# Optimization experiments

Hardware: AMD Instinct MI355X
Metric: run time of the kernel (lower is better)

## Reference

```python
import jax, jax.numpy as jnp
import numpy as np

D_X, D_K, D_V = 1024, 128, 128
B, N = 8, 2048


def setup_inputs() -> dict:
    key = jax.random.key(0)
    ks = jax.random.split(key, 7)
    s = lambda fan_in: 1.0 / np.sqrt(fan_in)
    return {
        "x": jax.random.normal(ks[0], (B, N, D_X), dtype=jnp.float32),
        "w_q": jax.random.uniform(ks[1], (D_K, D_X), jnp.float32, -s(D_X), s(D_X)),
        "b_q": jax.random.uniform(ks[2], (D_K,), jnp.float32, -s(D_X), s(D_X)),
        "w_k": jax.random.uniform(ks[3], (D_K, D_X), jnp.float32, -s(D_X), s(D_X)),
        "b_k": jax.random.uniform(ks[4], (D_K,), jnp.float32, -s(D_X), s(D_X)),
        "w_v": jax.random.uniform(ks[5], (D_V, D_X), jnp.float32, -s(D_X), s(D_X)),
        "b_v": jax.random.uniform(ks[6], (D_V,), jnp.float32, -s(D_X), s(D_X)),
    }


def reference(x, w_q, b_q, w_k, b_k, w_v, b_v):
    # Q is computed in the original module but unused; omit (no effect on output).
    K = jnp.einsum('bnx,kx->bnk', x, w_k) + b_k  # [B,N,d_k]
    V = jnp.einsum('bnx,vx->bnv', x, w_v) + b_v  # [B,N,d_v]
    # logits = K @ V^T / sqrt(d_k)  -> [B,N,N]  (note: K vs V, not Q vs K)
    scale = 1.0 / np.sqrt(D_K).astype(np.float32)
    logits = jnp.einsum('bnk,bmk->bnm', K, V) * scale
    attn = jax.nn.softmax(logits, axis=-1)
    return jnp.einsum('bnm,bmv->bnv', attn, V)
```

## Files before the change

### kernel.cpp

```cpp
#include <hip/hip_runtime.h>
#include <hip/hip_bf16.h>


typedef short s16x8 __attribute__((ext_vector_type(8)));
typedef float f32x4 __attribute__((ext_vector_type(4)));
typedef unsigned short u16;

#define AS1 __attribute__((address_space(1)))
#define AS3 __attribute__((address_space(3)))

__device__ __forceinline__ void gld_lds16(const void* g, void* l) {
  __builtin_amdgcn_global_load_lds((const AS1 unsigned int*)g, (AS3 unsigned int*)l, 16, 0, 0);
}

__device__ __forceinline__ float bf2f(u16 u) {
  unsigned int v = ((unsigned int)u) << 16;
  return __builtin_bit_cast(float, v);
}
__device__ __forceinline__ u16 f2bf(float f) {
  unsigned int u = __builtin_bit_cast(unsigned int, f);
  u += 0x7fffu + ((u >> 16) & 1u);
  return (u16)(u >> 16);
}
__device__ __forceinline__ unsigned pack_bf2(float a, float b) {
  unsigned ua = __builtin_bit_cast(unsigned, a) + 0x8000u;
  unsigned ub = __builtin_bit_cast(unsigned, b) + 0x8000u;
  return __builtin_amdgcn_perm(ub, ua, 0x07060302u);
}

__global__ __launch_bounds__(256, 4) void wconv_kernel(
    const float* __restrict__ wk, const float* __restrict__ wv,
    u16* __restrict__ wbf)
{
  const int e = (blockIdx.x * 256 + threadIdx.x) * 8;
  const float* src = (e < 131072) ? (wk + e) : (wv + (e - 131072));
  float4 a = *(const float4*)src;
  float4 b = *(const float4*)(src + 4);
  union { unsigned u[4]; s16x8 v; } pk;
  pk.u[0] = pack_bf2(a.x, a.y); pk.u[1] = pack_bf2(a.z, a.w);
  pk.u[2] = pack_bf2(b.x, b.y); pk.u[3] = pack_bf2(b.z, b.w);
  *(s16x8*)(wbf + e) = pk.v;
}

__global__ __launch_bounds__(256, 2) void kv_gemm_kernel(
    const float* __restrict__ x, const u16* __restrict__ wbf,
    const float* __restrict__ bk, const float* __restrict__ bv,
    u16* __restrict__ Kout, u16* __restrict__ Vout, u16* __restrict__ VTout)
{
  __shared__ u16 sA[2][4 * 512];
  __shared__ u16 sB[2][32 * 512];

  const int tid  = threadIdx.x;
  const int wave = tid >> 6;
  const int lane = tid & 63;
  const int l16  = lane & 15;
  const int lq   = lane >> 4;
  const int row0 = blockIdx.x * 32;

  f32x4 acc[2][4];
  for (int i = 0; i < 2; ++i)
    for (int j = 0; j < 4; ++j) acc[i][j] = (f32x4){0.f, 0.f, 0.f, 0.f};

  const int kc = tid & 7, arow = tid >> 3;
  const float* aSrc = x + (size_t)(row0 + arow) * 1024 + kc * 8;
  const int aSlot = ((((arow >> 4) * 2 + (kc >> 2)) * 64) + (kc & 3) * 16 + (arow & 15)) * 8;

  const u16* bSrc[8];
  for (int i = 0; i < 8; ++i) {
    const int sl = wave + i * 4;
    bSrc[i] = wbf + (size_t)((sl >> 1) * 16 + l16) * 1024 + (sl & 1) * 32 + lq * 8;
  }

  float4 p0a = *(const float4*)(aSrc);
  float4 p0b = *(const float4*)(aSrc + 4);
  float4 p1a = *(const float4*)(aSrc + 64);
  float4 p1b = *(const float4*)(aSrc + 68);
  for (int i = 0; i < 8; ++i)
    gld_lds16(bSrc[i], &sB[0][(wave + i * 4) * 512]);

  for (int s = 0; s < 16; ++s) {
    const int buf = s & 1;
    {
      union { unsigned u[4]; s16x8 v; } pk;
      pk.u[0] = pack_bf2(p0a.x, p0a.y); pk.u[1] = pack_bf2(p0a.z, p0a.w);
      pk.u[2] = pack_bf2(p0b.x, p0b.y); pk.u[3] = pack_bf2(p0b.z, p0b.w);
      *(s16x8*)(&sA[buf][aSlot]) = pk.v;
    }
    __syncthreads();
    if (s + 1 < 16)
      for (int i = 0; i < 8; ++i)
        gld_lds16(bSrc[i] + (s + 1) * 64, &sB[buf ^ 1][(wave + i * 4) * 512]);
    p0a = p1a; p0b = p1b;
    if (s + 2 < 16) {
      p1a = *(const float4*)(aSrc + (s + 2) * 64);
      p1b = *(const float4*)(aSrc + (s + 2) * 64 + 4);
    }
    s16x8 af[2][2], bf[4][2];
    for (int rb = 0; rb < 2; ++rb)
      for (int ks = 0; ks < 2; ++ks)
        af[rb][ks] = *(const s16x8*)(&sA[buf][((rb * 2 + ks) * 64 + lane) * 8]);
    for (int cb = 0; cb < 4; ++cb)
      for (int ks = 0; ks < 2; ++ks)
        bf[cb][ks] = *(const s16x8*)(&sB[buf][(((wave * 4 + cb) * 2 + ks) * 64 + lane) * 8]);
    for (int rb = 0; rb < 2; ++rb)
      for (int cb = 0; cb < 4; ++cb)
        for (int ks = 0; ks < 2; ++ks)
          acc[rb][cb] = __builtin_amdgcn_mfma_f32_16x16x32_bf16(af[rb][ks], bf[cb][ks], acc[rb][cb], 0, 0, 0);
  }

  const int  colBase = wave * 64;
  const bool isV = (wave >= 2);
  u16* outN = isV ? Vout : Kout;
  float fbias[4];
  for (int cb = 0; cb < 4; ++cb) {
    const int col = colBase + cb * 16 + l16;
    fbias[cb] = isV ? bv[col - 128] : bk[col];
  }
  for (int rb = 0; rb < 2; ++rb) {
    const int grow0 = row0 + rb * 16 + lq * 4;
    for (int cb = 0; cb < 4; ++cb) {
      const int gcol = colBase + cb * 16 + l16;
      const int ocol = isV ? (gcol - 128) : gcol;
      union { u16 u[4]; unsigned long long ull; } pk;
      for (int r = 0; r < 4; ++r) {
        u16 h = f2bf(acc[rb][cb][r] + fbias[cb]);
        outN[(size_t)(grow0 + r) * 128 + ocol] = h;
        pk.u[r] = h;
      }
      if (isV) {
        const int bidx = grow0 >> 11;
        const int n    = grow0 & 2047;
        *(unsigned long long*)(VTout + (size_t)bidx * 128 * 2048 + (size_t)ocol * 2048 + n) = pk.ull;
      }
    }
  }
}

__global__ __launch_bounds__(256, 2) void flash_kernel(
    const u16* __restrict__ Kmat, const u16* __restrict__ Vmat,
    const u16* __restrict__ VT, float* __restrict__ out,
    float* __restrict__ Opart, float* __restrict__ lbuf)
{
  __shared__ u16 sV[2][16 * 512];
  __shared__ u16 sVT[2][16 * 512];
  __shared__ u16 sP[64 * 66];

  const int tid  = threadIdx.x;
  const int wave = tid >> 6;
  const int lane = tid & 63;
  const int l16  = lane & 15;
  const int lq   = lane >> 4;
  const int b    = blockIdx.y;
  const int q0   = blockIdx.x * 64;
  const int z    = blockIdx.z;
  const int ntiles = (2048 / gridDim.z) / 64;
  const int mstart = z * (2048 / gridDim.z);
  const float scale = 0.08838834764831845f;

  s16x8 kf[4];
  {
    const u16* Kb = Kmat + ((size_t)b * 2048 + q0 + wave * 16 + l16) * 128 + lq * 8;
    for (int ks = 0; ks < 4; ++ks) kf[ks] = *(const s16x8*)(Kb + ks * 32);
  }

  const u16* vSrc[4];  const u16* vtSrc[4];
  {
    const u16* Vb  = Vmat + (size_t)b * 2048 * 128;
    const u16* VTb = VT   + (size_t)b * 128 * 2048;
    for (int i = 0; i < 4; ++i) {
      const int sl = wave + i * 4;
      vSrc[i]  = Vb  + (size_t)((sl >> 2) * 16 + l16) * 128 + (sl & 3) * 32 + lq * 8;
      vtSrc[i] = VTb + (size_t)((sl >> 1) * 16 + l16) * 2048 + (sl & 1) * 32 + lq * 8;
    }
  }

  f32x4 oacc[8];
  for (int v = 0; v < 8; ++v) oacc[v] = (f32x4){0.f, 0.f, 0.f, 0.f};
  float lrow[4] = {0.f, 0.f, 0.f, 0.f};

  for (int i = 0; i < 4; ++i) {
    gld_lds16(vSrc[i] + (size_t)mstart * 128, &sV[0][(wave + i * 4) * 512]);
    gld_lds16(vtSrc[i] + mstart,              &sVT[0][(wave + i * 4) * 512]);
  }

  for (int mt = 0; mt < ntiles; ++mt) {
    const int buf = mt & 1;
    __syncthreads();
    if (mt + 1 < ntiles) {
      const int m1 = mstart + (mt + 1) * 64;
      for (int i = 0; i < 4; ++i) {
        gld_lds16(vSrc[i] + (size_t)m1 * 128, &sV[buf ^ 1][(wave + i * 4) * 512]);
        gld_lds16(vtSrc[i] + m1,              &sVT[buf ^ 1][(wave + i * 4) * 512]);
      }
    }

    f32x4 sacc[4];
    for (int t = 0; t < 4; ++t) sacc[t] = (f32x4){0.f, 0.f, 0.f, 0.f};
    for (int ks = 0; ks < 4; ++ks)
      for (int t = 0; t < 4; ++t)
        sacc[t] = __builtin_amdgcn_mfma_f32_16x16x32_bf16(
            kf[ks], *(const s16x8*)(&sV[buf][(t * 4 + ks) * 512 + lane * 8]), sacc[t], 0, 0, 0);

    for (int r = 0; r < 4; ++r) {
      const int prow = (wave * 16 + lq * 4 + r) * 66;
      float rs = 0.f;
      for (int t = 0; t < 4; ++t) {
        float p = __expf(sacc[t][r] * scale);
        u16 h = f2bf(p);
        sP[prow + t * 16 + l16] = h;
        rs += bf2f(h);
      }
      lrow[r] += rs;
    }

    for (int ksm = 0; ksm < 2; ++ksm) {
      s16x8 a = *(const s16x8*)(&sP[(wave * 16 + l16) * 66 + ksm * 32 + lq * 8]);
      for (int v = 0; v < 8; ++v)
        oacc[v] = __builtin_amdgcn_mfma_f32_16x16x32_bf16(
            a, *(const s16x8*)(&sVT[buf][(v * 2 + ksm) * 512 + lane * 8]), oacc[v], 0, 0, 0);
    }
  }

  for (int r = 0; r < 4; ++r) {
    lrow[r] += __shfl_xor(lrow[r], 1);
    lrow[r] += __shfl_xor(lrow[r], 2);
    lrow[r] += __shfl_xor(lrow[r], 4);
    lrow[r] += __shfl_xor(lrow[r], 8);
  }

  const size_t rowg = (size_t)b * 2048 + q0 + wave * 16;
  if (gridDim.z == 1) {
    for (int r = 0; r < 4; ++r) {
      const float inv = 1.f / lrow[r];
      for (int v = 0; v < 8; ++v)
        out[(rowg + lq * 4 + r) * 128 + v * 16 + l16] = oacc[v][r] * inv;
    }
  } else {
    float* Op = Opart + (size_t)z * 2097152;
    float* lp = lbuf + (size_t)z * 32768;
    for (int r = 0; r < 4; ++r)
      for (int v = 0; v < 8; ++v)
        Op[(rowg + lq * 4 + r) * 128 + v * 16 + l16] = oacc[v][r];
    if (l16 == 0)
      for (int r = 0; r < 4; ++r)
        lp[rowg + lq * 4 + r] = lrow[r];
  }
}

__global__ __launch_bounds__(256, 4) void combine_kernel(
    const float* __restrict__ Opart, const float* __restrict__ lbuf,
    float* __restrict__ out)
{
  const int idx = blockIdx.x * 256 + threadIdx.x;
  const int row = idx >> 5;
  const float4 o0 = ((const float4*)Opart)[idx];
  const float4 o1 = ((const float4*)(Opart + 2097152))[idx];
  const float inv = 1.f / (lbuf[row] + lbuf[32768 + row]);
  float4 o;
  o.x = (o0.x + o1.x) * inv;
  o.y = (o0.y + o1.y) * inv;
  o.z = (o0.z + o1.z) * inv;
  o.w = (o0.w + o1.w) * inv;
  ((float4*)out)[idx] = o;
}

extern "C" void kernel_launch(void* const* d_in, const int* in_sizes, int n_in,
                              void* d_out, int out_size, void* d_ws, size_t ws_size,
                              hipStream_t stream) {
  const float* x  = (const float*)d_in[0];
  const float* wk = (const float*)d_in[3];
  const float* bk = (const float*)d_in[4];
  const float* wv = (const float*)d_in[5];
  const float* bv = (const float*)d_in[6];

  u16* ws   = (u16*)d_ws;
  u16* wbf  = ws;
  u16* Kmat = ws + 262144;
  u16* Vmat = Kmat + (size_t)16384 * 128;
  u16* VTm  = Vmat + (size_t)16384 * 128;
  float* Opart = (float*)(VTm + (size_t)16384 * 128);
  float* lbuf  = Opart + 2 * 2097152;
  const bool split = ws_size >= (size_t)30200000;

  wconv_kernel<<<128, 256, 0, stream>>>(wk, wv, wbf);
  kv_gemm_kernel<<<512, 256, 0, stream>>>(x, wbf, bk, bv, Kmat, Vmat, VTm);
  if (split) {
    flash_kernel<<<dim3(32, 8, 2), 256, 0, stream>>>(Kmat, Vmat, VTm,
                                                     (float*)d_out, Opart, lbuf);
    combine_kernel<<<2048, 256, 0, stream>>>(Opart, lbuf, (float*)d_out);
  } else {
    flash_kernel<<<dim3(32, 8, 1), 256, 0, stream>>>(Kmat, Vmat, VTm,
                                                     (float*)d_out, Opart, lbuf);
  }
}
```

Measured before the change: 179.7 us.

## Widen KV GEMM tile to 64 rows and deepen weight prefetch pipeline

```diff
diff --git a/kernel.cpp b/kernel.cpp
--- a/kernel.cpp
+++ b/kernel.cpp
@@ -42,20 +42,22 @@
   *(s16x8*)(wbf + e) = pk.v;
 }
 
-__global__ __launch_bounds__(256, 2) void kv_gemm_kernel(
+__global__ __launch_bounds__(512, 2) void kv_gemm_kernel(
     const float* __restrict__ x, const u16* __restrict__ wbf,
     const float* __restrict__ bk, const float* __restrict__ bv,
     u16* __restrict__ Kout, u16* __restrict__ Vout, u16* __restrict__ VTout)
 {
-  __shared__ u16 sA[2][4 * 512];
-  __shared__ u16 sB[2][32 * 512];
+  __shared__ u16 sA[2][8 * 512];
+  __shared__ u16 sB[4][32 * 512];
 
   const int tid  = threadIdx.x;
   const int wave = tid >> 6;
   const int lane = tid & 63;
   const int l16  = lane & 15;
   const int lq   = lane >> 4;
-  const int row0 = blockIdx.x * 32;
+  const int row0 = blockIdx.x * 64;
+  const int wr   = wave >> 2;
+  const int wc   = wave & 3;
 
   f32x4 acc[2][4];
   for (int i = 0; i < 2; ++i)
@@ -63,53 +65,63 @@
 
   const int kc = tid & 7, arow = tid >> 3;
   const float* aSrc = x + (size_t)(row0 + arow) * 1024 + kc * 8;
-  const int aSlot = ((((arow >> 4) * 2 + (kc >> 2)) * 64) + (kc & 3) * 16 + (arow & 15)) * 8;
-
-  const u16* bSrc[8];
-  for (int i = 0; i < 8; ++i) {
-    const int sl = wave + i * 4;
+  const int aSlot = (((arow >> 4) * 2 + (kc >> 2)) * 512) + ((kc & 3) * 16 + (arow & 15)) * 8;
+
+  const u16* bSrc[4];
+  for (int i = 0; i < 4; ++i) {
+    const int sl = wave + i * 8;
     bSrc[i] = wbf + (size_t)((sl >> 1) * 16 + l16) * 1024 + (sl & 1) * 32 + lq * 8;
   }
 
+  for (int i = 0; i < 4; ++i)
+    gld_lds16(bSrc[i], &sB[0][(wave + i * 8) * 512]);
   float4 p0a = *(const float4*)(aSrc);
   float4 p0b = *(const float4*)(aSrc + 4);
+  for (int i = 0; i < 4; ++i)
+    gld_lds16(bSrc[i] + 64, &sB[1][(wave + i * 8) * 512]);
   float4 p1a = *(const float4*)(aSrc + 64);
   float4 p1b = *(const float4*)(aSrc + 68);
-  for (int i = 0; i < 8; ++i)
-    gld_lds16(bSrc[i], &sB[0][(wave + i * 4) * 512]);
-
+
+#pragma unroll
   for (int s = 0; s < 16; ++s) {
-    const int buf = s & 1;
+    const int buf2 = s & 1, buf4 = s & 3;
     {
       union { unsigned u[4]; s16x8 v; } pk;
       pk.u[0] = pack_bf2(p0a.x, p0a.y); pk.u[1] = pack_bf2(p0a.z, p0a.w);
       pk.u[2] = pack_bf2(p0b.x, p0b.y); pk.u[3] = pack_bf2(p0b.z, p0b.w);
-      *(s16x8*)(&sA[buf][aSlot]) = pk.v;
-    }
-    __syncthreads();
-    if (s + 1 < 16)
-      for (int i = 0; i < 8; ++i)
-        gld_lds16(bSrc[i] + (s + 1) * 64, &sB[buf ^ 1][(wave + i * 4) * 512]);
+      *(s16x8*)(&sA[buf2][aSlot]) = pk.v;
+    }
+    asm volatile("s_waitcnt lgkmcnt(0)" ::: "memory");
+    __builtin_amdgcn_s_barrier();
+    if (s == 15) asm volatile("s_waitcnt vmcnt(0)" ::: "memory");
+    else         asm volatile("s_waitcnt vmcnt(6)" ::: "memory");
+    __builtin_amdgcn_sched_barrier(0);
+
+    if (s + 2 < 16) {
+      for (int i = 0; i < 4; ++i)
+        gld_lds16(bSrc[i] + (s + 2) * 64, &sB[(s + 2) & 3][(wave + i * 8) * 512]);
+    }
     p0a = p1a; p0b = p1b;
     if (s + 2 < 16) {
       p1a = *(const float4*)(aSrc + (s + 2) * 64);
       p1b = *(const float4*)(aSrc + (s + 2) * 64 + 4);
     }
-    s16x8 af[2][2], bf[4][2];
+
+    s16x8 af[2][2], bfr[4][2];
     for (int rb = 0; rb < 2; ++rb)
       for (int ks = 0; ks < 2; ++ks)
-        af[rb][ks] = *(const s16x8*)(&sA[buf][((rb * 2 + ks) * 64 + lane) * 8]);
+        af[rb][ks] = *(const s16x8*)(&sA[buf2][(((wr * 2 + rb) * 2 + ks) * 64 + lane) * 8]);
     for (int cb = 0; cb < 4; ++cb)
       for (int ks = 0; ks < 2; ++ks)
-        bf[cb][ks] = *(const s16x8*)(&sB[buf][(((wave * 4 + cb) * 2 + ks) * 64 + lane) * 8]);
+        bfr[cb][ks] = *(const s16x8*)(&sB[buf4][(((wc * 4 + cb) * 2 + ks) * 64 + lane) * 8]);
     for (int rb = 0; rb < 2; ++rb)
       for (int cb = 0; cb < 4; ++cb)
         for (int ks = 0; ks < 2; ++ks)
-          acc[rb][cb] = __builtin_amdgcn_mfma_f32_16x16x32_bf16(af[rb][ks], bf[cb][ks], acc[rb][cb], 0, 0, 0);
-  }
-
-  const int  colBase = wave * 64;
-  const bool isV = (wave >= 2);
+          acc[rb][cb] = __builtin_amdgcn_mfma_f32_16x16x32_bf16(af[rb][ks], bfr[cb][ks], acc[rb][cb], 0, 0, 0);
+  }
+
+  const int  colBase = wc * 64;
+  const bool isV = (wc >= 2);
   u16* outN = isV ? Vout : Kout;
   float fbias[4];
   for (int cb = 0; cb < 4; ++cb) {
@@ -117,7 +129,7 @@
     fbias[cb] = isV ? bv[col - 128] : bk[col];
   }
   for (int rb = 0; rb < 2; ++rb) {
-    const int grow0 = row0 + rb * 16 + lq * 4;
+    const int grow0 = row0 + wr * 32 + rb * 16 + lq * 4;
     for (int cb = 0; cb < 4; ++cb) {
       const int gcol = colBase + cb * 16 + l16;
       const int ocol = isV ? (gcol - 128) : gcol;
@@ -283,7 +295,7 @@
   const bool split = ws_size >= (size_t)30200000;
 
   wconv_kernel<<<128, 256, 0, stream>>>(wk, wv, wbf);
-  kv_gemm_kernel<<<512, 256, 0, stream>>>(x, wbf, bk, bv, Kmat, Vmat, VTm);
+  kv_gemm_kernel<<<256, 512, 0, stream>>>(x, wbf, bk, bv, Kmat, Vmat, VTm);
   if (split) {
     flash_kernel<<<dim3(32, 8, 2), 256, 0, stream>>>(Kmat, Vmat, VTm,
                                                      (float*)d_out, Opart, lbuf);
```

Result: faster. 170.9 us (-4.9%).
